# Performance work log

Hardware: AMD Instinct MI355X
Metric: run time of the kernel (lower is better)

The kernel has to match this reference:

```python
import jax, jax.numpy as jnp
import numpy as np

N = 50000   # nodes
E = 800000  # edges (avg degree 16)
D = 128     # feature dim
H = 4       # heads
DH = D // H # head dim


def setup_inputs() -> dict:
    key = jax.random.key(0)
    ks = jax.random.split(key, 12)
    s = 1.0 / np.sqrt(D)
    return {
        "x": jax.random.normal(ks[0], (N, D), dtype=jnp.float32),
        "src": jax.random.randint(ks[1], (E,), 0, N, dtype=jnp.int32),
        "dst": jax.random.randint(ks[2], (E,), 0, N, dtype=jnp.int32),
        # input_linear: Linear(d, d)
        "W_in": jax.random.uniform(ks[3], (D, D), jnp.float32, -s, s),
        "b_in": jax.random.uniform(ks[4], (D,), jnp.float32, -s, s),
        # attn_linear_u: Linear(d, n_heads), attn_linear_v: Linear(d, n_heads, bias=False)
        "W_au": jax.random.uniform(ks[5], (D, H), jnp.float32, -s, s),
        "b_au": jax.random.uniform(ks[6], (H,), jnp.float32, -s, s),
        "W_av": jax.random.uniform(ks[7], (D, H), jnp.float32, -s, s),
        # FFN: Linear(d, d) -> ReLU -> Linear(d, d)  (dropout=0)
        "W_f1": jax.random.uniform(ks[8], (D, D), jnp.float32, -s, s),
        "b_f1": jax.random.uniform(ks[9], (D,), jnp.float32, -s, s),
        "W_f2": jax.random.uniform(ks[10], (D, D), jnp.float32, -s, s),
        "b_f2": jax.random.uniform(ks[11], (D,), jnp.float32, -s, s),
    }


def reference(x, src, dst, W_in, b_in, W_au, b_au, W_av, W_f1, b_f1, W_f2, b_f2):
    h = x @ W_in + b_in                                # [N, D]
    su = h @ W_au + b_au                               # [N, H]
    sv = h @ W_av                                      # [N, H]
    # u_add_v gather + LeakyReLU
    e = jax.nn.leaky_relu(su[src] + sv[dst], 0.2)      # [E, H]
    # edge_softmax: softmax over incoming edges of each dst node
    m = jax.ops.segment_max(e, dst, num_segments=N)    # [N, H]
    ex = jnp.exp(e - m[dst])                           # [E, H]
    z = jax.ops.segment_sum(ex, dst, num_segments=N)   # [N, H]
    p = ex / z[dst]                                    # [E, H]
    # u_mul_e_sum: weighted aggregation (note reshape order (N, d_head, H))
    hu = h.reshape(N, DH, H)[src]                      # [E, DH, H]
    agg = jax.ops.segment_sum(hu * p[:, None, :], dst, num_segments=N)  # [N, DH, H]
    y = agg.reshape(N, D)
    # FFN
    return jax.nn.relu(y @ W_f1 + b_f1) @ W_f2 + b_f2
```

## Files before the change

kernel.cpp:

```cpp
#include <hip/hip_runtime.h>
#include <hip/hip_bf16.h>
#include <math.h>

#define D 128
#define NHEADS 4

static constexpr int CAP  = 64;
static constexpr int CAPB = 5120;
static constexpr int EB   = 2048;

typedef __attribute__((ext_vector_type(8))) short bf16x8;
typedef __attribute__((ext_vector_type(4))) float f32x4;

__device__ __forceinline__ float4 ld4(const float* p) {
    return *reinterpret_cast<const float4*>(p);
}
__device__ __forceinline__ float4 fma4(float a, float4 b, float4 c) {
    c.x = fmaf(a, b.x, c.x); c.y = fmaf(a, b.y, c.y);
    c.z = fmaf(a, b.z, c.z); c.w = fmaf(a, b.w, c.w);
    return c;
}
__device__ __forceinline__ unsigned short f2bf(float f) {
    __hip_bfloat16 b = __float2bfloat16(f);
    return __builtin_bit_cast(unsigned short, b);
}
__device__ __forceinline__ float bf2f(unsigned short u) {
    return __uint_as_float((unsigned)u << 16);
}
__device__ __forceinline__ void cvt_hilo(const float4& a0, const float4& a1,
                                         bf16x8& hi, bf16x8& lo) {
    float v[8] = {a0.x, a0.y, a0.z, a0.w, a1.x, a1.y, a1.z, a1.w};
#pragma unroll
    for (int i = 0; i < 8; ++i) {
        unsigned short h = f2bf(v[i]);
        hi[i] = (short)h;
        lo[i] = (short)f2bf(v[i] - bf2f(h));
    }
}

__global__ __launch_bounds__(256)
void clear_kernel(int* __restrict__ bucket_cnt, int nb16) {
    for (int i = threadIdx.x; i < nb16; i += 256) bucket_cnt[i] = 0;
}

template<bool OUT16, bool RELU, bool A16>
__global__ __launch_bounds__(256)
void mfma_gemm128(const float* __restrict__ Af, const unsigned short* __restrict__ A16p,
                  const float* __restrict__ W,
                  const float* __restrict__ bias, float* __restrict__ out,
                  unsigned short* __restrict__ out16, int N, int ntiles)
{
    __shared__ unsigned short wh[D * D];
    __shared__ unsigned short wl[D * D];

    const int t = threadIdx.x;
#pragma unroll
    for (int i = 0; i < 16; ++i) {
        int g = t + i * 256;
        int col = g & 127;
        int k0 = (g >> 7) << 2;
        short4 h4, l4;
#pragma unroll
        for (int k = 0; k < 4; ++k) {
            float v = W[(size_t)(k0 + k) * D + col];
            unsigned short hb = f2bf(v);
            ((short*)&h4)[k] = (short)hb;
            ((short*)&l4)[k] = (short)f2bf(v - bf2f(hb));
        }
        int off = col * D + (k0 ^ ((col & 7) << 3));
        *reinterpret_cast<short4*>(&wh[off]) = h4;
        *reinterpret_cast<short4*>(&wl[off]) = l4;
    }
    __syncthreads();

    const int wid  = t >> 6;
    const int lane = t & 63;
    const int q8   = (lane >> 4) * 8;

    for (int tile = blockIdx.x; tile < ntiles; tile += gridDim.x) {
        const int rbase = tile * 64 + wid * 16;
        const int arow  = rbase + (lane & 15);

        bf16x8 ahi[4], alo[4];
#pragma unroll
        for (int ks = 0; ks < 4; ++ks) {
            if constexpr (A16) {
                bf16x8 z;
#pragma unroll
                for (int i = 0; i < 8; ++i) z[i] = 0;
                ahi[ks] = (arow < N)
                    ? *reinterpret_cast<const bf16x8*>(A16p + (size_t)arow * D + 32 * ks + q8)
                    : z;
            } else {
                float4 a0 = {0, 0, 0, 0}, a1 = {0, 0, 0, 0};
                if (arow < N) {
                    const float* ap = Af + (size_t)arow * D + 32 * ks + q8;
                    a0 = ld4(ap); a1 = ld4(ap + 4);
                }
                cvt_hilo(a0, a1, ahi[ks], alo[ks]);
            }
        }

        f32x4 acc[8];
#pragma unroll
        for (int ct = 0; ct < 8; ++ct) acc[ct] = (f32x4){0.f, 0.f, 0.f, 0.f};

#pragma unroll
        for (int ct = 0; ct < 8; ++ct) {
            const int colb = ct * 16 + (lane & 15);
            const int sw   = (colb & 7) << 3;
            bf16x8 bh[4], bl[4];
#pragma unroll
            for (int ks = 0; ks < 4; ++ks) {
                int off = colb * D + ((32 * ks + q8) ^ sw);
                bh[ks] = *reinterpret_cast<const bf16x8*>(&wh[off]);
                bl[ks] = *reinterpret_cast<const bf16x8*>(&wl[off]);
            }
#pragma unroll
            for (int ks = 0; ks < 4; ++ks) {
                acc[ct] = __builtin_amdgcn_mfma_f32_16x16x32_bf16(ahi[ks], bh[ks], acc[ct], 0, 0, 0);
                acc[ct] = __builtin_amdgcn_mfma_f32_16x16x32_bf16(ahi[ks], bl[ks], acc[ct], 0, 0, 0);
                if constexpr (!A16)
                    acc[ct] = __builtin_amdgcn_mfma_f32_16x16x32_bf16(alo[ks], bh[ks], acc[ct], 0, 0, 0);
            }
        }

        const int crow0 = rbase + (lane >> 4) * 4;
#pragma unroll
        for (int ct = 0; ct < 8; ++ct) {
            const int col = ct * 16 + (lane & 15);
            const float bv = bias[col];
#pragma unroll
            for (int j = 0; j < 4; ++j) {
                const int r = crow0 + j;
                if (r < N) {
                    float v = acc[ct][j] + bv;
                    if constexpr (RELU) v = fmaxf(v, 0.f);
                    if constexpr (OUT16)
                        out16[(size_t)r * D + col] = f2bf(v);
                    else
                        out[(size_t)r * D + col] = v;
                }
            }
        }
    }
}

__global__ __launch_bounds__(256)
void bin_kernel(const int* __restrict__ src, const int* __restrict__ dst,
                int* __restrict__ bucket_cnt ,
                unsigned* __restrict__ bucket_buf, int E, int NB)
{
    __shared__ int hist[256];
    __shared__ int base[256];
    __shared__ int off[256];
    const int t = threadIdx.x;
    hist[t] = 0; off[t] = 0;
    __syncthreads();

    const int e0 = blockIdx.x * EB;
#pragma unroll
    for (int j = 0; j < EB / 256; ++j) {
        int idx = e0 + j * 256 + t;
        if (idx < E) atomicAdd(&hist[dst[idx] >> 8], 1);
    }
    __syncthreads();
    if (t < NB) {
        int hv = hist[t];
        base[t] = hv ? atomicAdd(&bucket_cnt[t * 16], hv) : 0;
    }
    __syncthreads();
#pragma unroll
    for (int j = 0; j < EB / 256; ++j) {
        int idx = e0 + j * 256 + t;
        if (idx < E) {
            int d = dst[idx];
            int b = d >> 8;
            int p = base[b] + atomicAdd(&off[b], 1);
            if (p < CAPB)
                bucket_buf[(size_t)b * CAPB + p] =
                    (unsigned)(src[idx] | ((d & 255) << 16));
        }
    }
}

__global__ __launch_bounds__(256)
void csr_att_kernel(const int* __restrict__ bucket_cnt, const unsigned* __restrict__ bucket_buf,
                    unsigned short* __restrict__ slot, int* __restrict__ deg, int N, int NB,
                    const unsigned short* __restrict__ h16,
                    const float* __restrict__ Wau, const float* __restrict__ bau,
                    const float* __restrict__ Wav,
                    float* __restrict__ su, float* __restrict__ sv)
{
    __shared__ unsigned ebuf[CAPB];
    __shared__ int cur[256];

    const int t = threadIdx.x;
    if ((int)blockIdx.x < NB) {
        const int b = blockIdx.x;
        const int cnt = min(bucket_cnt[b * 16], CAPB);
        cur[t] = 0;
        for (int i = t; i < cnt; i += 256)
            ebuf[i] = bucket_buf[(size_t)b * CAPB + i];
        __syncthreads();
        for (int i = t; i < cnt; i += 256) {
            unsigned e = ebuf[i];
            int dl = e >> 16;
            int pos = atomicAdd(&cur[dl], 1);
            if (pos < CAP)
                slot[(((size_t)(b * 256 + dl)) << 6) + pos] = (unsigned short)(e & 0xffff);
        }
        __syncthreads();
        int n = b * 256 + t;
        if (n < N) deg[n] = min(cur[t], CAP);
        return;
    }

    const int wid  = t >> 6;
    const int lane = t & 63;
    const int n = (blockIdx.x - NB) * 4 + wid;
    if (n >= N) return;

    const int c = lane * 2;
    unsigned u = *reinterpret_cast<const unsigned*>(h16 + (size_t)n * D + c);
    const float hx = __uint_as_float(u << 16);
    const float hy = __uint_as_float(u & 0xffff0000u);

    float4 s_u = {0, 0, 0, 0}, s_v = {0, 0, 0, 0};
    s_u = fma4(hx, ld4(Wau + c * NHEADS), s_u);
    s_u = fma4(hy, ld4(Wau + (c + 1) * NHEADS), s_u);
    s_v = fma4(hx, ld4(Wav + c * NHEADS), s_v);
    s_v = fma4(hy, ld4(Wav + (c + 1) * NHEADS), s_v);

#pragma unroll
    for (int d2 = 1; d2 < 64; d2 <<= 1) {
        s_u.x += __shfl_xor(s_u.x, d2); s_u.y += __shfl_xor(s_u.y, d2);
        s_u.z += __shfl_xor(s_u.z, d2); s_u.w += __shfl_xor(s_u.w, d2);
        s_v.x += __shfl_xor(s_v.x, d2); s_v.y += __shfl_xor(s_v.y, d2);
        s_v.z += __shfl_xor(s_v.z, d2); s_v.w += __shfl_xor(s_v.w, d2);
    }
    if (lane == 0) {
        float4 ub = ld4(bau);
        s_u.x += ub.x; s_u.y += ub.y; s_u.z += ub.z; s_u.w += ub.w;
        *reinterpret_cast<float4*>(su + (size_t)n * NHEADS) = s_u;
        *reinterpret_cast<float4*>(sv + (size_t)n * NHEADS) = s_v;
    }
}

__global__ __launch_bounds__(256)
void agg_kernel(const unsigned short* __restrict__ h16, const float* __restrict__ su,
                const float* __restrict__ sv, const int* __restrict__ deg_arr,
                const unsigned short* __restrict__ slot, float* __restrict__ y, int N)
{
    __shared__ int   s_s[4][64];
    __shared__ float s_p[4][64][4];

    const int wslot = threadIdx.x >> 6;
    const int lane  = threadIdx.x & 63;
    const int n = blockIdx.x * 4 + wslot;
    if (n >= N) return;

    const int deg = deg_arr[n];

    if (deg == 0) {
        *reinterpret_cast<float2*>(y + (size_t)n * D + lane * 2) = float2{0.f, 0.f};
        return;
    }

    const float4 sv4 = ld4(sv + (size_t)n * NHEADS);
    const int psel = (lane & 1) * 2;

    int sj = 0;
    float4 ex4 = {0.f, 0.f, 0.f, 0.f};
    if (lane < deg) {
        sj = slot[((size_t)n << 6) + lane];
        float4 u = ld4(su + (size_t)sj * NHEADS);
        float e0 = u.x + sv4.x, e1 = u.y + sv4.y, e2 = u.z + sv4.z, e3 = u.w + sv4.w;
        e0 = e0 >= 0.f ? e0 : 0.2f * e0; e1 = e1 >= 0.f ? e1 : 0.2f * e1;
        e2 = e2 >= 0.f ? e2 : 0.2f * e2; e3 = e3 >= 0.f ? e3 : 0.2f * e3;
        ex4.x = __expf(e0); ex4.y = __expf(e1);
        ex4.z = __expf(e2); ex4.w = __expf(e3);
    }
    float4 z4 = ex4;
#pragma unroll
    for (int d2 = 1; d2 < 64; d2 <<= 1) {
        z4.x += __shfl_xor(z4.x, d2); z4.y += __shfl_xor(z4.y, d2);
        z4.z += __shfl_xor(z4.z, d2); z4.w += __shfl_xor(z4.w, d2);
    }

    s_s[wslot][lane] = sj;
    *reinterpret_cast<float4*>(&s_p[wslot][lane][0]) = ex4;
    __builtin_amdgcn_wave_barrier();

    float2 acc = {0.f, 0.f};
    for (int j0 = 0; j0 < deg; j0 += 16) {
        const int je = (deg - j0 < 16) ? (deg - j0) : 16;
        unsigned hv[16];
        float2   pv[16];
#pragma unroll
        for (int k = 0; k < 16; ++k) {
            if (k < je) {
                int s = s_s[wslot][j0 + k];
                hv[k] = *reinterpret_cast<const unsigned*>(h16 + ((size_t)s << 7) + (lane << 1));
                pv[k] = *reinterpret_cast<const float2*>(&s_p[wslot][j0 + k][psel]);
            }
        }
#pragma unroll
        for (int k = 0; k < 16; ++k) {
            if (k < je) {
                acc.x = fmaf(pv[k].x, __uint_as_float(hv[k] << 16), acc.x);
                acc.y = fmaf(pv[k].y, __uint_as_float(hv[k] & 0xffff0000u), acc.y);
            }
        }
    }

    const float2 z2 = (lane & 1) ? float2{z4.z, z4.w} : float2{z4.x, z4.y};
    float2 o;
    o.x = acc.x / z2.x;
    o.y = acc.y / z2.y;
    *reinterpret_cast<float2*>(y + (size_t)n * D + lane * 2) = o;
}

extern "C" void kernel_launch(void* const* d_in, const int* in_sizes, int n_in,
                              void* d_out, int out_size, void* d_ws, size_t ws_size,
                              hipStream_t stream) {
    const float* x    = (const float*)d_in[0];
    const int*   src  = (const int*)d_in[1];
    const int*   dst  = (const int*)d_in[2];
    const float* W_in = (const float*)d_in[3];
    const float* b_in = (const float*)d_in[4];
    const float* W_au = (const float*)d_in[5];
    const float* b_au = (const float*)d_in[6];
    const float* W_av = (const float*)d_in[7];
    const float* W_f1 = (const float*)d_in[8];
    const float* b_f1 = (const float*)d_in[9];
    const float* W_f2 = (const float*)d_in[10];
    const float* b_f2 = (const float*)d_in[11];
    float* out = (float*)d_out;

    const int N = in_sizes[0] / D;
    const int E = in_sizes[1];
    const int NB = (N + 255) / 256;

    char* ws = (char*)d_ws;
    size_t o = 0;
    auto alloc = [&](size_t bytes) -> void* {
        void* p = ws + o;
        o += (bytes + 255) & ~(size_t)255;
        return p;
    };
    unsigned short* h16        = (unsigned short*)alloc((size_t)N * D * 2);
    unsigned short* hid16      = (unsigned short*)alloc((size_t)N * D * 2);
    float*          y          = (float*)alloc((size_t)N * D * 4);
    float*          su         = (float*)alloc((size_t)N * NHEADS * 4);
    float*          sv         = (float*)alloc((size_t)N * NHEADS * 4);
    int*            bucket_cnt = (int*)alloc((size_t)NB * 16 * 4);
    unsigned*       bucket_buf = (unsigned*)alloc((size_t)NB * CAPB * 4);
    unsigned short* slot       = (unsigned short*)alloc((size_t)NB * 256 * CAP * 2);
    int*            deg        = (int*)alloc((size_t)N * 4);

    const int bgrid  = (E + EB - 1) / EB;
    const int ntiles = (N + 63) / 64;
    const int ggrid  = (ntiles + 1) / 2;
    const int agrid  = (N + 3) / 4;

    clear_kernel<<<1, 256, 0, stream>>>(bucket_cnt, NB * 16);

    bin_kernel<<<bgrid, 256, 0, stream>>>(src, dst, bucket_cnt, bucket_buf, E, NB);

    mfma_gemm128<true, false, false><<<ggrid, 256, 0, stream>>>(
        x, nullptr, W_in, b_in, nullptr, h16, N, ntiles);

    csr_att_kernel<<<NB + agrid, 256, 0, stream>>>(bucket_cnt, bucket_buf, slot, deg, N, NB,
                                                   h16, W_au, b_au, W_av, su, sv);

    agg_kernel<<<agrid, 256, 0, stream>>>(h16, su, sv, deg, slot, y, N);

    mfma_gemm128<true, true, false><<<ggrid, 256, 0, stream>>>(
        y, nullptr, W_f1, b_f1, nullptr, hid16, N, ntiles);

    mfma_gemm128<false, false, true><<<ggrid, 256, 0, stream>>>(
        nullptr, hid16, W_f2, b_f2, out, nullptr, N, ntiles);
}
```

Measured before the change: 143.7 us.

## Process four edges per wave with 16-byte gathers in aggregation kernel

The aggregation kernel now splits each 64-lane wave into four 16-lane groups. Each group handles a different incoming edge per iteration and loads 8 bf16 features (16 bytes) per lane instead of 2, with a shuffle reduction across groups at the end. This widens memory transactions and cuts loop iterations, so more independent gathers are in flight per instruction. In exchange it drops the 16-deep explicit prefetch unrolling, adds cross-group shuffles, and writes output from only a quarter of the lanes.

```diff
diff --git a/kernel.cpp b/kernel.cpp
--- a/kernel.cpp
+++ b/kernel.cpp
@@ -27,6 +27,9 @@
 __device__ __forceinline__ float bf2f(unsigned short u) {
     return __uint_as_float((unsigned)u << 16);
 }
+__device__ __forceinline__ float bflo(unsigned u) { return __uint_as_float(u << 16); }
+__device__ __forceinline__ float bfhi(unsigned u) { return __uint_as_float(u & 0xffff0000u); }
+
 __device__ __forceinline__ void cvt_hilo(const float4& a0, const float4& a1,
                                          bf16x8& hi, bf16x8& lo) {
     float v[8] = {a0.x, a0.y, a0.z, a0.w, a1.x, a1.y, a1.z, a1.w};
@@ -223,8 +226,8 @@
 
     const int c = lane * 2;
     unsigned u = *reinterpret_cast<const unsigned*>(h16 + (size_t)n * D + c);
-    const float hx = __uint_as_float(u << 16);
-    const float hy = __uint_as_float(u & 0xffff0000u);
+    const float hx = bflo(u);
+    const float hy = bfhi(u);
 
     float4 s_u = {0, 0, 0, 0}, s_v = {0, 0, 0, 0};
     s_u = fma4(hx, ld4(Wau + c * NHEADS), s_u);
@@ -261,14 +264,19 @@
     if (n >= N) return;
 
     const int deg = deg_arr[n];
+    const int l15 = lane & 15;
+    const int grp = lane >> 4;
 
     if (deg == 0) {
-        *reinterpret_cast<float2*>(y + (size_t)n * D + lane * 2) = float2{0.f, 0.f};
+        if (grp == 0) {
+            float4 zz = {0.f, 0.f, 0.f, 0.f};
+            *reinterpret_cast<float4*>(y + (size_t)n * D + l15 * 8) = zz;
+            *reinterpret_cast<float4*>(y + (size_t)n * D + l15 * 8 + 4) = zz;
+        }
         return;
     }
 
     const float4 sv4 = ld4(sv + (size_t)n * NHEADS);
-    const int psel = (lane & 1) * 2;
 
     int sj = 0;
     float4 ex4 = {0.f, 0.f, 0.f, 0.f};
@@ -292,33 +300,44 @@
     *reinterpret_cast<float4*>(&s_p[wslot][lane][0]) = ex4;
     __builtin_amdgcn_wave_barrier();
 
-    float2 acc = {0.f, 0.f};
-    for (int j0 = 0; j0 < deg; j0 += 16) {
-        const int je = (deg - j0 < 16) ? (deg - j0) : 16;
-        unsigned hv[16];
-        float2   pv[16];
-#pragma unroll
-        for (int k = 0; k < 16; ++k) {
-            if (k < je) {
-                int s = s_s[wslot][j0 + k];
-                hv[k] = *reinterpret_cast<const unsigned*>(h16 + ((size_t)s << 7) + (lane << 1));
-                pv[k] = *reinterpret_cast<const float2*>(&s_p[wslot][j0 + k][psel]);
-            }
-        }
-#pragma unroll
-        for (int k = 0; k < 16; ++k) {
-            if (k < je) {
-                acc.x = fmaf(pv[k].x, __uint_as_float(hv[k] << 16), acc.x);
-                acc.y = fmaf(pv[k].y, __uint_as_float(hv[k] & 0xffff0000u), acc.y);
-            }
-        }
-    }
-
-    const float2 z2 = (lane & 1) ? float2{z4.z, z4.w} : float2{z4.x, z4.y};
-    float2 o;
-    o.x = acc.x / z2.x;
-    o.y = acc.y / z2.y;
-    *reinterpret_cast<float2*>(y + (size_t)n * D + lane * 2) = o;
+    float4 accA = {0.f, 0.f, 0.f, 0.f};
+    float4 accB = {0.f, 0.f, 0.f, 0.f};
+    for (int j0 = 0; j0 < deg; j0 += 4) {
+        const int j = j0 + grp;
+        uint4  hv = {0u, 0u, 0u, 0u};
+        float4 p4 = {0.f, 0.f, 0.f, 0.f};
+        if (j < deg) {
+            int s = s_s[wslot][j];
+            hv = *reinterpret_cast<const uint4*>(h16 + ((size_t)s << 7) + l15 * 8);
+            p4 = *reinterpret_cast<const float4*>(&s_p[wslot][j][0]);
+        }
+        accA.x = fmaf(p4.x, bflo(hv.x), accA.x);
+        accA.y = fmaf(p4.y, bfhi(hv.x), accA.y);
+        accA.z = fmaf(p4.z, bflo(hv.y), accA.z);
+        accA.w = fmaf(p4.w, bfhi(hv.y), accA.w);
+        accB.x = fmaf(p4.x, bflo(hv.z), accB.x);
+        accB.y = fmaf(p4.y, bfhi(hv.z), accB.y);
+        accB.z = fmaf(p4.z, bflo(hv.w), accB.z);
+        accB.w = fmaf(p4.w, bfhi(hv.w), accB.w);
+    }
+
+#pragma unroll
+    for (int d2 = 16; d2 < 64; d2 <<= 1) {
+        accA.x += __shfl_xor(accA.x, d2); accA.y += __shfl_xor(accA.y, d2);
+        accA.z += __shfl_xor(accA.z, d2); accA.w += __shfl_xor(accA.w, d2);
+        accB.x += __shfl_xor(accB.x, d2); accB.y += __shfl_xor(accB.y, d2);
+        accB.z += __shfl_xor(accB.z, d2); accB.w += __shfl_xor(accB.w, d2);
+    }
+
+    if (grp == 0) {
+        float4 oA, oB;
+        oA.x = accA.x / z4.x; oA.y = accA.y / z4.y;
+        oA.z = accA.z / z4.z; oA.w = accA.w / z4.w;
+        oB.x = accB.x / z4.x; oB.y = accB.y / z4.y;
+        oB.z = accB.z / z4.z; oB.w = accB.w / z4.w;
+        *reinterpret_cast<float4*>(y + (size_t)n * D + l15 * 8)     = oA;
+        *reinterpret_cast<float4*>(y + (size_t)n * D + l15 * 8 + 4) = oB;
+    }
 }
 
 extern "C" void kernel_launch(void* const* d_in, const int* in_sizes, int n_in,
```

Result: no change. 143.4 us (-0.2%).
